# Kernel optimization log

Measured on AMD Instinct MI355X. Metric: run time of the kernel, lower is better.

Reference implementation:

```python
import jax, jax.numpy as jnp
import numpy as np

B, C, H, W = 32, 512, 32, 32  # in_dims = token_dim = 512, num_heads = 1
D = 512  # token_dim * num_heads
EPS = 1e-12  # torch F.normalize eps


def l2norm(x, axis):
    n = jnp.sqrt(jnp.sum(x * x, axis=axis, keepdims=True))
    return x / jnp.maximum(n, EPS)


def setup_inputs() -> dict:
    key = jax.random.key(0)
    ks = jax.random.split(key, 10)
    s = 1.0 / np.sqrt(D)
    return {
        "x_4d": jax.random.normal(ks[0], (B, C, H, W), dtype=jnp.float32),
        "Wq": jax.random.uniform(ks[1], (D, D), jnp.float32, -s, s),
        "bq": jax.random.uniform(ks[2], (D,), jnp.float32, -s, s),
        "Wk": jax.random.uniform(ks[3], (D, D), jnp.float32, -s, s),
        "bk": jax.random.uniform(ks[4], (D,), jnp.float32, -s, s),
        "w_g": jax.random.normal(ks[5], (D, 1), dtype=jnp.float32),
        "Wp": jax.random.uniform(ks[6], (D, D), jnp.float32, -s, s),
        "bp": jax.random.uniform(ks[7], (D,), jnp.float32, -s, s),
        "Wf": jax.random.uniform(ks[8], (D, D), jnp.float32, -s, s),
        "bf": jax.random.uniform(ks[9], (D,), jnp.float32, -s, s),
    }


def reference(x_4d, Wq, bq, Wk, bk, w_g, Wp, bp, Wf, bf):
    b, c, h, w = x_4d.shape
    n = h * w
    scale = D ** (-0.5)
    x = x_4d.reshape(b, c, n).transpose(0, 2, 1)  # [b, n, c]
    query = l2norm(jnp.einsum("bnc,dc->bnd", x, Wq) + bq, axis=-1)  # [b, n, d]
    key = l2norm(jnp.einsum("bnc,dc->bnd", x, Wk) + bk, axis=-1)    # [b, n, d]
    query_weight = query @ w_g                      # [b, n, 1]
    a = l2norm(query_weight * scale, axis=1)        # normalize over sequence dim
    g = jnp.sum(a * query, axis=1)                  # [b, d] global context
    out = jnp.einsum("bnd,ed->bne", g[:, None, :] * key, Wp) + bp + query
    out = jnp.einsum("bnd,ed->bne", out, Wf) + bf
    return out.transpose(0, 2, 1).reshape(b, c, h, w)
```

## Files before the change

### kernel.cpp

```cpp
#include <hip/hip_runtime.h>
#include <math.h>

#define B_ 32
#define D_ 512
#define N_ 1024
#define T_ 32768
#define SCALE 0.04419417382415922f

typedef unsigned short u16;
typedef __attribute__((ext_vector_type(8))) short bf16x8;
typedef __attribute__((ext_vector_type(4))) float f32x4;
typedef __attribute__((ext_vector_type(8))) unsigned short u16x8;

__device__ __forceinline__ u16 bf16_rn(float f) {
    unsigned u = __float_as_uint(f);
    u += 0x7FFFu + ((u >> 16) & 1u);
    return (u16)(u >> 16);
}
__device__ __forceinline__ float bf16f(u16 h) {
    return __uint_as_float(((unsigned)h) << 16);
}

__device__ __forceinline__ void g2l16(const u16* g, u16* lds) {
    __builtin_amdgcn_global_load_lds(
        (const __attribute__((address_space(1))) unsigned int*)g,
        (__attribute__((address_space(3))) unsigned int*)lds, 16, 0, 0);
}

__device__ __forceinline__ float waveRedSum(float v) {
#pragma unroll
    for (int off = 32; off > 0; off >>= 1) v += __shfl_xor(v, off, 64);
    return v;
}


__global__ __launch_bounds__(256) void convw_k(const float* __restrict__ W0,
                                               const float* __restrict__ W1,
                                               const float* __restrict__ W2,
                                               u16* O0, u16* O1, u16* O2) {
    const int s = blockIdx.y;
    const float* src = (s == 0) ? W0 : ((s == 1) ? W1 : W2);
    u16* O = (s == 0) ? O0 : ((s == 1) ? O1 : O2);
    const size_t i0 = (size_t)blockIdx.x * 2048 + threadIdx.x * 8;
    u16 o[8];
#pragma unroll
    for (int j = 0; j < 8; ++j) o[j] = bf16_rn(src[i0 + j]);
    *(u16x8*)&O[i0] = *(const u16x8*)&o[0];
}


__global__ __launch_bounds__(256) void finalize_k(float* __restrict__ ssqQ,
                                                  float* __restrict__ ssqK,
                                                  float* __restrict__ qwr,
                                                  float* __restrict__ Sb) {
    __shared__ float red[4];
    const int i = blockIdx.x * 256 + threadIdx.x;
    const float rq = 1.f / fmaxf(sqrtf(ssqQ[i]), 1e-12f);
    ssqQ[i] = rq;
    const float rk = 1.f / fmaxf(sqrtf(ssqK[i]), 1e-12f);
    ssqK[i] = rk;
    const float qwp = qwr[i] * rq;
    qwr[i] = qwp * rq;
    float s = qwp * qwp;
    s = waveRedSum(s);
    if ((threadIdx.x & 63) == 0) red[threadIdx.x >> 6] = s;
    __syncthreads();
    if (threadIdx.x == 0)
        atomicAdd(Sb + (blockIdx.x >> 2), red[0] + red[1] + red[2] + red[3]);
}

__global__ __launch_bounds__(512) void gctx_k(const float* __restrict__ qw,
                                              const u16* __restrict__ Qn,
                                              float* __restrict__ g) {
    const int b = blockIdx.y;
    const int n0 = blockIdx.x * 128;
    const int d = threadIdx.x;
    const u16* qp = Qn + ((size_t)b * N_ + n0) * D_ + d;
    const float* wp = qw + (size_t)b * N_ + n0;
    float acc = 0.f;
    for (int n = 0; n < 128; ++n) acc += wp[n] * bf16f(qp[(size_t)n * D_]);
    atomicAdd(g + b * D_ + d, acc);
}

__global__ __launch_bounds__(256) void scalewp_k(const float* __restrict__ Wp,
                                                 const float* __restrict__ g,
                                                 const float* __restrict__ Sb,
                                                 u16* __restrict__ WpG) {
    const int b = blockIdx.y;
    const float fb = SCALE / fmaxf(SCALE * sqrtf(Sb[b]), 1e-12f);
    const size_t f0 = (size_t)blockIdx.x * 2048 + threadIdx.x * 8;
    const int c = (int)(f0 & 511);
    u16 o[8];
#pragma unroll
    for (int j = 0; j < 8; ++j)
        o[j] = bf16_rn(Wp[f0 + j] * g[b * D_ + c + j] * fb);
    *(u16x8*)&WpG[(size_t)b * 262144 + f0] = *(const u16x8*)&o[0];
}

__global__ __launch_bounds__(512, 4) void mgemm0(
        const float* __restrict__ x, const u16* __restrict__ B0,
        const u16* __restrict__ B1,
        const float* __restrict__ bias0, const float* __restrict__ bias1,
        const float* __restrict__ wg,
        float* __restrict__ ssqQ, float* __restrict__ ssqK,
        float* __restrict__ qwr, u16* uout0, u16* uout1) {
    __shared__ u16 As[128 * 72];
    __shared__ u16 Bs[256 * 64];
    const int tid = threadIdx.x;
    const int l = tid & 63, w = tid >> 6;
    const int gid = blockIdx.x;
    const int xcd = gid & 7;
    const int bx = (gid >> 3) & 3;
    const int by = (gid >> 5) * 8 + xcd;
    const int t0 = by * 128;
    const bool sel = bx >= 2;
    const int e0 = (bx & 1) * 256;
    const u16* B = sel ? B1 : B0;
    const float* bias = sel ? bias1 : bias0;
    u16* uout = sel ? uout1 : uout0;
    float* ssq = sel ? ssqK : ssqQ;

    const int tr = tid & 127;
    const int csl = (tid >> 7) * 16;
    const float* xrow = x + (((size_t)((t0 >> 10) * D_ + csl)) << 10) +
                        (t0 & 1023) + tr;
    size_t gB[4];
    u16* ldsB[4];
#pragma unroll
    for (int i = 0; i < 4; ++i) {
        const int rr = w * 32 + i * 8 + (l >> 3);
        gB[i] = (size_t)(e0 + rr) * 512 + (((l & 7) ^ (rr & 7)) * 8);
        ldsB[i] = Bs + (w * 32 + i * 8) * 64;
    }

    const int wr = w >> 2, wc = w & 3, kg = l >> 4, r16 = l & 15;
    int aoff[4][2], boff[4][2];
#pragma unroll
    for (int f = 0; f < 4; ++f)
#pragma unroll
        for (int h = 0; h < 2; ++h) {
            const int ra = wr * 64 + f * 16 + r16;
            aoff[f][h] = ra * 72 + (h * 4 + kg) * 8;
            const int rb = wc * 64 + f * 16 + r16;
            boff[f][h] = rb * 64 + (((h * 4 + kg) ^ (rb & 7)) * 8);
        }

    f32x4 acc[4][4];
#pragma unroll
    for (int i = 0; i < 4; ++i)
#pragma unroll
        for (int j = 0; j < 4; ++j) acc[i][j] = 0.f;

    float ar[16];
#pragma unroll
    for (int j = 0; j < 16; ++j) ar[j] = xrow[(size_t)j << 10];

#pragma unroll 1
    for (int s = 0; s < 8; ++s) {
        const int c0 = s * 64;
        __syncthreads();
        u16 pk[16];
#pragma unroll
        for (int j = 0; j < 16; ++j) pk[j] = bf16_rn(ar[j]);
        *(u16x8*)&As[tr * 72 + csl]     = *(const u16x8*)&pk[0];
        *(u16x8*)&As[tr * 72 + csl + 8] = *(const u16x8*)&pk[8];
#pragma unroll
        for (int i = 0; i < 4; ++i) g2l16(B + gB[i] + c0, ldsB[i]);
        if (s < 7) {
#pragma unroll
            for (int j = 0; j < 16; ++j)
                ar[j] = xrow[(size_t)(c0 + 64 + j) << 10];
        }
        __syncthreads();
#pragma unroll
        for (int h = 0; h < 2; ++h) {
            bf16x8 av[4], bv[4];
#pragma unroll
            for (int f = 0; f < 4; ++f) {
                av[f] = *(const bf16x8*)&As[aoff[f][h]];
                bv[f] = *(const bf16x8*)&Bs[boff[f][h]];
            }
#pragma unroll
            for (int i = 0; i < 4; ++i)
#pragma unroll
                for (int j = 0; j < 4; ++j)
                    acc[i][j] = __builtin_amdgcn_mfma_f32_16x16x32_bf16(
                        av[i], bv[j], acc[i][j], 0, 0, 0);
        }
    }

    const int mb = wr * 64 + kg * 4;
    const int nb = wc * 64 + r16;
    float bb[4], wgv[4];
#pragma unroll
    for (int fn = 0; fn < 4; ++fn) {
        const int n = e0 + nb + fn * 16;
        bb[fn] = bias[n];
        wgv[fn] = sel ? 0.f : wg[n];
    }
#pragma unroll
    for (int fm = 0; fm < 4; ++fm) {
#pragma unroll
        for (int q = 0; q < 4; ++q) {
            const int m = t0 + mb + fm * 16 + q;
            float s2 = 0.f, wd = 0.f;
#pragma unroll
            for (int fn = 0; fn < 4; ++fn) {
                const float val = acc[fm][fn][q] + bb[fn];
                uout[(size_t)m * 512 + e0 + nb + fn * 16] = bf16_rn(val);
                s2 += val * val;
                wd += val * wgv[fn];
            }
#pragma unroll
            for (int off = 1; off < 16; off <<= 1) {
                s2 += __shfl_xor(s2, off, 64);
                wd += __shfl_xor(wd, off, 64);
            }
            if (r16 == 0) {
                atomicAdd(ssq + m, s2);
                if (!sel) atomicAdd(qwr + m, wd);
            }
        }
    }
}

template <int MODE>
__global__ __launch_bounds__(256) void mgemm12(
        const u16* __restrict__ A, const u16* __restrict__ B0,
        const float* __restrict__ bias,
        const float* __restrict__ rsA, const float* __restrict__ rsQ,
        u16* uout, float* __restrict__ fout) {
    __shared__ u16 As[128 * 64];
    __shared__ u16 Bs[128 * 64];
    const int tid = threadIdx.x;
    const int l = tid & 63, w = tid >> 6;
    const int gid = blockIdx.x;
    const int xcd = gid & 7;

    int rowt, col, batch;
    if (MODE == 1) {
        const int j = gid >> 3;
        batch = (j >> 5) * 8 + xcd;
        const int r = j & 31;
        rowt = batch * 8 + (r >> 2);
        col = r & 3;
    } else {
        col = (gid >> 3) & 3;
        rowt = (gid >> 5) * 8 + xcd;
        batch = rowt >> 3;
    }
    const int tt0 = rowt * 128;
    const int e0 = col * 128;
    const u16* B = (MODE == 1) ? B0 + (size_t)batch * 262144 : B0;
    const int arow0 = (MODE == 2) ? e0 : tt0;
    const int brow0 = (MODE == 2) ? tt0 : e0;

    size_t gA[4], gB[4];
    u16 *ldsA[4], *ldsB[4];
#pragma unroll
    for (int i = 0; i < 4; ++i) {
        const int rr = w * 32 + i * 8 + (l >> 3);
        const int sw = ((l & 7) ^ (rr & 7)) * 8;
        gA[i] = (size_t)(arow0 + rr) * 512 + sw;
        gB[i] = (size_t)(brow0 + rr) * 512 + sw;
        ldsA[i] = As + (w * 32 + i * 8) * 64;
        ldsB[i] = Bs + (w * 32 + i * 8) * 64;
    }

    const int wr = w >> 1, wc = w & 1, kg = l >> 4, r16 = l & 15;
    int aoff[4][2], boff[4][2];
#pragma unroll
    for (int f = 0; f < 4; ++f)
#pragma unroll
        for (int h = 0; h < 2; ++h) {
            const int ra = wr * 64 + f * 16 + r16;
            aoff[f][h] = ra * 64 + (((h * 4 + kg) ^ (ra & 7)) * 8);
            const int rb = wc * 64 + f * 16 + r16;
            boff[f][h] = rb * 64 + (((h * 4 + kg) ^ (rb & 7)) * 8);
        }

    f32x4 acc[4][4];
#pragma unroll
    for (int i = 0; i < 4; ++i)
#pragma unroll
        for (int j = 0; j < 4; ++j) acc[i][j] = 0.f;

#pragma unroll 1
    for (int c0 = 0; c0 < 512; c0 += 64) {
        __syncthreads();
#pragma unroll
        for (int i = 0; i < 4; ++i) {
            g2l16(A + gA[i] + c0, ldsA[i]);
            g2l16(B + gB[i] + c0, ldsB[i]);
        }
        __syncthreads();
#pragma unroll
        for (int h = 0; h < 2; ++h) {
            bf16x8 av[4], bv[4];
#pragma unroll
            for (int f = 0; f < 4; ++f) {
                av[f] = *(const bf16x8*)&As[aoff[f][h]];
                bv[f] = *(const bf16x8*)&Bs[boff[f][h]];
            }
#pragma unroll
            for (int i = 0; i < 4; ++i)
#pragma unroll
                for (int j = 0; j < 4; ++j)
                    acc[i][j] = __builtin_amdgcn_mfma_f32_16x16x32_bf16(
                        av[i], bv[j], acc[i][j], 0, 0, 0);
        }
    }

    const int mb = wr * 64 + kg * 4;
    const int nb = wc * 64 + r16;
    if (MODE == 1) {
#pragma unroll
        for (int fm = 0; fm < 4; ++fm) {
            const int m0 = tt0 + mb + fm * 16;
            const float4 ra4 = *(const float4*)(rsA + m0);
            const float4 rq4 = *(const float4*)(rsQ + m0);
            const float ra_[4] = {ra4.x, ra4.y, ra4.z, ra4.w};
            const float rq_[4] = {rq4.x, rq4.y, rq4.z, rq4.w};
#pragma unroll
            for (int fn = 0; fn < 4; ++fn) {
                const int n = e0 + nb + fn * 16;
                const float bb = bias[n];
#pragma unroll
                for (int q = 0; q < 4; ++q) {
                    const size_t idx = (size_t)(m0 + q) * 512 + n;
                    const float val = acc[fm][fn][q] * ra_[q] + bb +
                                      bf16f(uout[idx]) * rq_[q];
                    uout[idx] = bf16_rn(val);
                }
            }
        }
    } else {
#pragma unroll
        for (int fm = 0; fm < 4; ++fm)
#pragma unroll
            for (int fn = 0; fn < 4; ++fn) {
                const int ntok = (tt0 & 1023) + nb + fn * 16;
#pragma unroll
                for (int q = 0; q < 4; ++q) {
                    const int e = e0 + mb + fm * 16 + q;
                    fout[((size_t)(batch * D_ + e) << 10) + ntok] =
                        acc[fm][fn][q] + bias[e];
                }
            }
    }
}


extern "C" void kernel_launch(void* const* d_in, const int* in_sizes, int n_in,
                              void* d_out, int out_size, void* d_ws, size_t ws_size,
                              hipStream_t stream) {
    const float* x  = (const float*)d_in[0];
    const float* Wq = (const float*)d_in[1];
    const float* bq = (const float*)d_in[2];
    const float* Wk = (const float*)d_in[3];
    const float* bk = (const float*)d_in[4];
    const float* wg = (const float*)d_in[5];
    const float* Wp = (const float*)d_in[6];
    const float* bp = (const float*)d_in[7];
    const float* Wf = (const float*)d_in[8];
    const float* bf = (const float*)d_in[9];
    float* out = (float*)d_out;

    char* Wb = (char*)d_ws;
    u16* WpG = (u16*)Wb;
    u16* Qn  = (u16*)(Wb + 33554432ull);
    u16* Kn  = (u16*)(Wb + 67108864ull);
    char* S  = Wb + 100663296ull;
    u16* Wqbf = (u16*)S;
    u16* Wkbf = (u16*)(S + 524288ull);
    u16* Wfbf = (u16*)(S + 1048576ull);
    char* Z   = S + 1572864ull;
    float* SSQQ = (float*)Z;
    float* SSQK = (float*)(Z + 131072ull);
    float* QWR  = (float*)(Z + 262144ull);
    float* G    = (float*)(Z + 393216ull);
    float* Sb   = (float*)(Z + 458752ull);
    const size_t ZBYTES = 458752ull + 128ull;

    const dim3 blk(256);

    convw_k<<<dim3(128, 3), blk, 0, stream>>>(Wq, Wk, Wf, Wqbf, Wkbf, Wfbf);
    hipMemsetAsync(Z, 0, ZBYTES, stream);
    mgemm0<<<dim3(1024), dim3(512), 0, stream>>>(x, Wqbf, Wkbf, bq, bk, wg,
                                                 SSQQ, SSQK, QWR, Qn, Kn);
    finalize_k<<<dim3(128), blk, 0, stream>>>(SSQQ, SSQK, QWR, Sb);
    gctx_k<<<dim3(8, B_), dim3(512), 0, stream>>>(QWR, Qn, G);
    scalewp_k<<<dim3(128, B_), blk, 0, stream>>>(Wp, G, Sb, WpG);
    mgemm12<1><<<dim3(1024), blk, 0, stream>>>(Kn, WpG, bp, SSQK, SSQQ, Qn,
                                               nullptr);
    mgemm12<2><<<dim3(1024), blk, 0, stream>>>(Wfbf, Qn, bf, nullptr, nullptr,
                                               nullptr, out);
}
```

Measured before the change: 149.5 us.

## Unify GEMM kernels with double-buffered LDS and 512-thread 128x128 tiles

Merges the three GEMM kernels into one templated kernel. Each uses 512 threads on a 128x128 tile (each wave computes 32x64) with double-buffered LDS, so the global-to-LDS loads for the next K-step overlap the current MFMA work and only one barrier is needed per step. The first GEMM moves from 128x256 tiles to 128x128, which doubles its grid to 2048 blocks, and its A tile now uses an XOR swizzle instead of padding. The costs are more LDS per block (two buffers each for A and B) and less register-level reuse per wave.

```diff
diff --git a/kernel.cpp b/kernel.cpp
--- a/kernel.cpp
+++ b/kernel.cpp
@@ -97,226 +97,195 @@
     *(u16x8*)&WpG[(size_t)b * 262144 + f0] = *(const u16x8*)&o[0];
 }
 
-__global__ __launch_bounds__(512, 4) void mgemm0(
-        const float* __restrict__ x, const u16* __restrict__ B0,
-        const u16* __restrict__ B1,
+template <int MODE>
+__global__ __launch_bounds__(512, 4) void mg(
+        const float* __restrict__ x, const u16* __restrict__ Ag,
+        const u16* __restrict__ B0, const u16* __restrict__ B1,
         const float* __restrict__ bias0, const float* __restrict__ bias1,
         const float* __restrict__ wg,
         float* __restrict__ ssqQ, float* __restrict__ ssqK,
-        float* __restrict__ qwr, u16* uout0, u16* uout1) {
-    __shared__ u16 As[128 * 72];
-    __shared__ u16 Bs[256 * 64];
+        float* __restrict__ qwr,
+        const float* __restrict__ rsA, const float* __restrict__ rsQ,
+        u16* uout0, u16* uout1, float* __restrict__ fout) {
+    __shared__ u16 As[2][128 * 64];
+    __shared__ u16 Bs[2][128 * 64];
     const int tid = threadIdx.x;
     const int l = tid & 63, w = tid >> 6;
-    const int gid = blockIdx.x;
-    const int xcd = gid & 7;
-    const int bx = (gid >> 3) & 3;
-    const int by = (gid >> 5) * 8 + xcd;
-    const int t0 = by * 128;
-    const bool sel = bx >= 2;
-    const int e0 = (bx & 1) * 256;
-    const u16* B = sel ? B1 : B0;
-    const float* bias = sel ? bias1 : bias0;
-    u16* uout = sel ? uout1 : uout0;
-    float* ssq = sel ? ssqK : ssqQ;
-
+    const int gid = blockIdx.x, xcd = gid & 7;
+
+    int t0, e0, batch;
+    bool sel = false;
+    if (MODE == 0) {
+        const int bx = (gid >> 3) & 7;
+        const int by = (gid >> 6) * 8 + xcd;
+        t0 = by * 128; sel = bx >= 4; e0 = (bx & 3) * 128; batch = by >> 3;
+    } else if (MODE == 1) {
+        const int j = gid >> 3;
+        batch = (j >> 5) * 8 + xcd;
+        const int r = j & 31;
+        t0 = (batch * 8 + (r >> 2)) * 128;
+        e0 = (r & 3) * 128;
+    } else {
+        e0 = ((gid >> 3) & 3) * 128;
+        const int rowt = (gid >> 5) * 8 + xcd;
+        t0 = rowt * 128; batch = rowt >> 3;
+    }
+    const u16* B = (MODE == 0) ? (sel ? B1 : B0)
+                 : (MODE == 1) ? B0 + (size_t)batch * 262144 : B0;
+    const float* bias = (MODE == 0) ? (sel ? bias1 : bias0) : bias0;
+    u16* uout = (MODE == 0) ? (sel ? uout1 : uout0) : uout0;
+    const int arow0 = (MODE == 2) ? e0 : t0;
+    const int brow0 = (MODE == 2) ? t0 : e0;
+
+    size_t gA[2], gB[2];
+    int lAB[2];
+#pragma unroll
+    for (int i = 0; i < 2; ++i) {
+        const int rr = w * 16 + i * 8 + (l >> 3);
+        const int sw = ((l & 7) ^ (rr & 7)) * 8;
+        gA[i] = (size_t)(arow0 + rr) * 512 + sw;
+        gB[i] = (size_t)(brow0 + rr) * 512 + sw;
+        lAB[i] = (w * 16 + i * 8) * 64;
+    }
     const int tr = tid & 127;
-    const int csl = (tid >> 7) * 16;
-    const float* xrow = x + (((size_t)((t0 >> 10) * D_ + csl)) << 10) +
-                        (t0 & 1023) + tr;
-    size_t gB[4];
-    u16* ldsB[4];
-#pragma unroll
-    for (int i = 0; i < 4; ++i) {
-        const int rr = w * 32 + i * 8 + (l >> 3);
-        gB[i] = (size_t)(e0 + rr) * 512 + (((l & 7) ^ (rr & 7)) * 8);
-        ldsB[i] = Bs + (w * 32 + i * 8) * 64;
-    }
-
-    const int wr = w >> 2, wc = w & 3, kg = l >> 4, r16 = l & 15;
-    int aoff[4][2], boff[4][2];
+    const int ch0 = (tid >> 7) * 2;
+    const float* xrow = nullptr;
+    int wA0 = 0, wA1 = 0;
+    if (MODE == 0) {
+        xrow = x + (((size_t)(batch * D_ + ch0 * 8)) << 10) + (t0 & 1023) + tr;
+        wA0 = tr * 64 + ((ch0 ^ (tr & 7)) * 8);
+        wA1 = tr * 64 + (((ch0 + 1) ^ (tr & 7)) * 8);
+    }
+
+    const int wr = w >> 1, wc = w & 1, kg = l >> 4, r16 = l & 15;
+    int aoff[2][2], boff[4][2];
+#pragma unroll
+    for (int f = 0; f < 2; ++f)
+#pragma unroll
+        for (int h = 0; h < 2; ++h) {
+            const int ra = wr * 32 + f * 16 + r16;
+            aoff[f][h] = ra * 64 + (((h * 4 + kg) ^ (ra & 7)) * 8);
+        }
 #pragma unroll
     for (int f = 0; f < 4; ++f)
 #pragma unroll
         for (int h = 0; h < 2; ++h) {
-            const int ra = wr * 64 + f * 16 + r16;
-            aoff[f][h] = ra * 72 + (h * 4 + kg) * 8;
             const int rb = wc * 64 + f * 16 + r16;
             boff[f][h] = rb * 64 + (((h * 4 + kg) ^ (rb & 7)) * 8);
         }
 
-    f32x4 acc[4][4];
-#pragma unroll
-    for (int i = 0; i < 4; ++i)
+    f32x4 acc[2][4];
+#pragma unroll
+    for (int i = 0; i < 2; ++i)
 #pragma unroll
         for (int j = 0; j < 4; ++j) acc[i][j] = 0.f;
 
     float ar[16];
-#pragma unroll
-    for (int j = 0; j < 16; ++j) ar[j] = xrow[(size_t)j << 10];
-
+    if (MODE == 0) {
+#pragma unroll
+        for (int j = 0; j < 16; ++j) ar[j] = xrow[(size_t)j << 10];
+    }
+#pragma unroll
+    for (int i = 0; i < 2; ++i) g2l16(B + gB[i], &Bs[0][lAB[i]]);
+    if (MODE != 0) {
+#pragma unroll
+        for (int i = 0; i < 2; ++i) g2l16(Ag + gA[i], &As[0][lAB[i]]);
+    } else {
+        u16 pk[16];
+#pragma unroll
+        for (int j = 0; j < 16; ++j) pk[j] = bf16_rn(ar[j]);
+        *(u16x8*)&As[0][wA0] = *(const u16x8*)&pk[0];
+        *(u16x8*)&As[0][wA1] = *(const u16x8*)&pk[8];
+#pragma unroll
+        for (int j = 0; j < 16; ++j) ar[j] = xrow[(size_t)(64 + j) << 10];
+    }
+    __syncthreads();
+
+    int cur = 0;
 #pragma unroll 1
     for (int s = 0; s < 8; ++s) {
-        const int c0 = s * 64;
-        __syncthreads();
-        u16 pk[16];
-#pragma unroll
-        for (int j = 0; j < 16; ++j) pk[j] = bf16_rn(ar[j]);
-        *(u16x8*)&As[tr * 72 + csl]     = *(const u16x8*)&pk[0];
-        *(u16x8*)&As[tr * 72 + csl + 8] = *(const u16x8*)&pk[8];
-#pragma unroll
-        for (int i = 0; i < 4; ++i) g2l16(B + gB[i] + c0, ldsB[i]);
+        const int nxt = cur ^ 1;
         if (s < 7) {
-#pragma unroll
-            for (int j = 0; j < 16; ++j)
-                ar[j] = xrow[(size_t)(c0 + 64 + j) << 10];
-        }
-        __syncthreads();
+            const int cn = (s + 1) * 64;
+#pragma unroll
+            for (int i = 0; i < 2; ++i) g2l16(B + gB[i] + cn, &Bs[nxt][lAB[i]]);
+            if (MODE != 0) {
+#pragma unroll
+                for (int i = 0; i < 2; ++i)
+                    g2l16(Ag + gA[i] + cn, &As[nxt][lAB[i]]);
+            }
+        }
 #pragma unroll
         for (int h = 0; h < 2; ++h) {
-            bf16x8 av[4], bv[4];
-#pragma unroll
-            for (int f = 0; f < 4; ++f) {
-                av[f] = *(const bf16x8*)&As[aoff[f][h]];
-                bv[f] = *(const bf16x8*)&Bs[boff[f][h]];
-            }
-#pragma unroll
-            for (int i = 0; i < 4; ++i)
+            bf16x8 av[2], bv[4];
+#pragma unroll
+            for (int f = 0; f < 2; ++f)
+                av[f] = *(const bf16x8*)&As[cur][aoff[f][h]];
+#pragma unroll
+            for (int f = 0; f < 4; ++f)
+                bv[f] = *(const bf16x8*)&Bs[cur][boff[f][h]];
+#pragma unroll
+            for (int i = 0; i < 2; ++i)
 #pragma unroll
                 for (int j = 0; j < 4; ++j)
                     acc[i][j] = __builtin_amdgcn_mfma_f32_16x16x32_bf16(
                         av[i], bv[j], acc[i][j], 0, 0, 0);
         }
-    }
-
-    const int mb = wr * 64 + kg * 4;
+        if (MODE == 0 && s < 7) {
+            u16 pk[16];
+#pragma unroll
+            for (int j = 0; j < 16; ++j) pk[j] = bf16_rn(ar[j]);
+            *(u16x8*)&As[nxt][wA0] = *(const u16x8*)&pk[0];
+            *(u16x8*)&As[nxt][wA1] = *(const u16x8*)&pk[8];
+            if (s < 6) {
+#pragma unroll
+                for (int j = 0; j < 16; ++j)
+                    ar[j] = xrow[(size_t)((s + 2) * 64 + j) << 10];
+            }
+        }
+        __syncthreads();
+        cur = nxt;
+    }
+
+    const int mb = wr * 32 + kg * 4;
     const int nb = wc * 64 + r16;
-    float bb[4], wgv[4];
-#pragma unroll
-    for (int fn = 0; fn < 4; ++fn) {
-        const int n = e0 + nb + fn * 16;
-        bb[fn] = bias[n];
-        wgv[fn] = sel ? 0.f : wg[n];
-    }
-#pragma unroll
-    for (int fm = 0; fm < 4; ++fm) {
-#pragma unroll
-        for (int q = 0; q < 4; ++q) {
-            const int m = t0 + mb + fm * 16 + q;
-            float s2 = 0.f, wd = 0.f;
-#pragma unroll
-            for (int fn = 0; fn < 4; ++fn) {
-                const float val = acc[fm][fn][q] + bb[fn];
-                uout[(size_t)m * 512 + e0 + nb + fn * 16] = bf16_rn(val);
-                s2 += val * val;
-                wd += val * wgv[fn];
-            }
-#pragma unroll
-            for (int off = 1; off < 16; off <<= 1) {
-                s2 += __shfl_xor(s2, off, 64);
-                wd += __shfl_xor(wd, off, 64);
-            }
-            if (r16 == 0) {
-                atomicAdd(ssq + m, s2);
-                if (!sel) atomicAdd(qwr + m, wd);
-            }
-        }
-    }
-}
-
-template <int MODE>
-__global__ __launch_bounds__(256) void mgemm12(
-        const u16* __restrict__ A, const u16* __restrict__ B0,
-        const float* __restrict__ bias,
-        const float* __restrict__ rsA, const float* __restrict__ rsQ,
-        u16* uout, float* __restrict__ fout) {
-    __shared__ u16 As[128 * 64];
-    __shared__ u16 Bs[128 * 64];
-    const int tid = threadIdx.x;
-    const int l = tid & 63, w = tid >> 6;
-    const int gid = blockIdx.x;
-    const int xcd = gid & 7;
-
-    int rowt, col, batch;
-    if (MODE == 1) {
-        const int j = gid >> 3;
-        batch = (j >> 5) * 8 + xcd;
-        const int r = j & 31;
-        rowt = batch * 8 + (r >> 2);
-        col = r & 3;
-    } else {
-        col = (gid >> 3) & 3;
-        rowt = (gid >> 5) * 8 + xcd;
-        batch = rowt >> 3;
-    }
-    const int tt0 = rowt * 128;
-    const int e0 = col * 128;
-    const u16* B = (MODE == 1) ? B0 + (size_t)batch * 262144 : B0;
-    const int arow0 = (MODE == 2) ? e0 : tt0;
-    const int brow0 = (MODE == 2) ? tt0 : e0;
-
-    size_t gA[4], gB[4];
-    u16 *ldsA[4], *ldsB[4];
-#pragma unroll
-    for (int i = 0; i < 4; ++i) {
-        const int rr = w * 32 + i * 8 + (l >> 3);
-        const int sw = ((l & 7) ^ (rr & 7)) * 8;
-        gA[i] = (size_t)(arow0 + rr) * 512 + sw;
-        gB[i] = (size_t)(brow0 + rr) * 512 + sw;
-        ldsA[i] = As + (w * 32 + i * 8) * 64;
-        ldsB[i] = Bs + (w * 32 + i * 8) * 64;
-    }
-
-    const int wr = w >> 1, wc = w & 1, kg = l >> 4, r16 = l & 15;
-    int aoff[4][2], boff[4][2];
-#pragma unroll
-    for (int f = 0; f < 4; ++f)
-#pragma unroll
-        for (int h = 0; h < 2; ++h) {
-            const int ra = wr * 64 + f * 16 + r16;
-            aoff[f][h] = ra * 64 + (((h * 4 + kg) ^ (ra & 7)) * 8);
-            const int rb = wc * 64 + f * 16 + r16;
-            boff[f][h] = rb * 64 + (((h * 4 + kg) ^ (rb & 7)) * 8);
-        }
-
-    f32x4 acc[4][4];
-#pragma unroll
-    for (int i = 0; i < 4; ++i)
-#pragma unroll
-        for (int j = 0; j < 4; ++j) acc[i][j] = 0.f;
-
-#pragma unroll 1
-    for (int c0 = 0; c0 < 512; c0 += 64) {
-        __syncthreads();
-#pragma unroll
-        for (int i = 0; i < 4; ++i) {
-            g2l16(A + gA[i] + c0, ldsA[i]);
-            g2l16(B + gB[i] + c0, ldsB[i]);
-        }
-        __syncthreads();
-#pragma unroll
-        for (int h = 0; h < 2; ++h) {
-            bf16x8 av[4], bv[4];
-#pragma unroll
-            for (int f = 0; f < 4; ++f) {
-                av[f] = *(const bf16x8*)&As[aoff[f][h]];
-                bv[f] = *(const bf16x8*)&Bs[boff[f][h]];
-            }
-#pragma unroll
-            for (int i = 0; i < 4; ++i)
-#pragma unroll
-                for (int j = 0; j < 4; ++j)
-                    acc[i][j] = __builtin_amdgcn_mfma_f32_16x16x32_bf16(
-                        av[i], bv[j], acc[i][j], 0, 0, 0);
-        }
-    }
-
-    const int mb = wr * 64 + kg * 4;
-    const int nb = wc * 64 + r16;
-    if (MODE == 1) {
-#pragma unroll
-        for (int fm = 0; fm < 4; ++fm) {
-            const int m0 = tt0 + mb + fm * 16;
+    if (MODE == 0) {
+        float bb[4], wgv[4];
+#pragma unroll
+        for (int fn = 0; fn < 4; ++fn) {
+            const int n = e0 + nb + fn * 16;
+            bb[fn] = bias[n];
+            wgv[fn] = sel ? 0.f : wg[n];
+        }
+        float* ssq = sel ? ssqK : ssqQ;
+#pragma unroll
+        for (int fm = 0; fm < 2; ++fm) {
+#pragma unroll
+            for (int q = 0; q < 4; ++q) {
+                const int m = t0 + mb + fm * 16 + q;
+                float s2 = 0.f, wd = 0.f;
+#pragma unroll
+                for (int fn = 0; fn < 4; ++fn) {
+                    const float val = acc[fm][fn][q] + bb[fn];
+                    uout[(size_t)m * 512 + e0 + nb + fn * 16] = bf16_rn(val);
+                    s2 += val * val;
+                    wd += val * wgv[fn];
+                }
+#pragma unroll
+                for (int off = 1; off < 16; off <<= 1) {
+                    s2 += __shfl_xor(s2, off, 64);
+                    wd += __shfl_xor(wd, off, 64);
+                }
+                if (r16 == 0) {
+                    atomicAdd(ssq + m, s2);
+                    if (!sel) atomicAdd(qwr + m, wd);
+                }
+            }
+        }
+    } else if (MODE == 1) {
+#pragma unroll
+        for (int fm = 0; fm < 2; ++fm) {
+            const int m0 = t0 + mb + fm * 16;
             const float4 ra4 = *(const float4*)(rsA + m0);
             const float4 rq4 = *(const float4*)(rsQ + m0);
             const float ra_[4] = {ra4.x, ra4.y, ra4.z, ra4.w};
@@ -336,10 +305,10 @@
         }
     } else {
 #pragma unroll
-        for (int fm = 0; fm < 4; ++fm)
+        for (int fm = 0; fm < 2; ++fm)
 #pragma unroll
             for (int fn = 0; fn < 4; ++fn) {
-                const int ntok = (tt0 & 1023) + nb + fn * 16;
+                const int ntok = (t0 & 1023) + nb + fn * 16;
 #pragma unroll
                 for (int q = 0; q < 4; ++q) {
                     const int e = e0 + mb + fm * 16 + q;
@@ -386,13 +355,18 @@
 
     convw_k<<<dim3(128, 3), blk, 0, stream>>>(Wq, Wk, Wf, Wqbf, Wkbf, Wfbf);
     hipMemsetAsync(Z, 0, ZBYTES, stream);
-    mgemm0<<<dim3(1024), dim3(512), 0, stream>>>(x, Wqbf, Wkbf, bq, bk, wg,
-                                                 SSQQ, SSQK, QWR, Qn, Kn);
+    mg<0><<<dim3(2048), dim3(512), 0, stream>>>(x, nullptr, Wqbf, Wkbf, bq, bk,
+                                                wg, SSQQ, SSQK, QWR, nullptr,
+                                                nullptr, Qn, Kn, nullptr);
     finalize_k<<<dim3(128), blk, 0, stream>>>(SSQQ, SSQK, QWR, Sb);
     gctx_k<<<dim3(8, B_), dim3(512), 0, stream>>>(QWR, Qn, G);
     scalewp_k<<<dim3(128, B_), blk, 0, stream>>>(Wp, G, Sb, WpG);
-    mgemm12<1><<<dim3(1024), blk, 0, stream>>>(Kn, WpG, bp, SSQK, SSQQ, Qn,
-                                               nullptr);
-    mgemm12<2><<<dim3(1024), blk, 0, stream>>>(Wfbf, Qn, bf, nullptr, nullptr,
-                                               nullptr, out);
-}
+    mg<1><<<dim3(1024), dim3(512), 0, stream>>>(nullptr, Kn, WpG, nullptr, bp,
+                                                nullptr, nullptr, nullptr,
+                                                nullptr, nullptr, SSQK, SSQQ,
+                                                Qn, nullptr, nullptr);
+    mg<2><<<dim3(1024), dim3(512), 0, stream>>>(nullptr, Wfbf, Qn, nullptr, bf,
+                                                nullptr, nullptr, nullptr,
+                                                nullptr, nullptr, nullptr,
+                                                nullptr, Qn, nullptr, out);
+}
```

Result: slower. 162.4 us (+8.6%).
